# Kernel optimization log

Measured on AMD Instinct MI355X. Metric: run time of the kernel, lower is better.

Reference implementation:

```python
import jax, jax.numpy as jnp
import numpy as np

N_NODES = 100000
D_FEAT = 128            # per-embedding width; concat of 4 -> 512
INPUT_DIM = 4 * D_FEAT
HIDDEN_DIM = 64
N_SAMPLES = 250000


def _glorot(key, fan_in, fan_out):
    r = np.sqrt(6.0 / fan_in).astype(np.float32)
    return jax.random.uniform(key, (fan_in, fan_out), minval=-r, maxval=r, dtype=jnp.float32)


def setup_inputs() -> dict:
    key = jax.random.key(0)
    k1, k2, k3, k4, k5 = jax.random.split(key, 5)
    input1 = jax.random.normal(k1, (N_NODES, D_FEAT), dtype=jnp.float32)
    input2 = jax.random.normal(k2, (N_NODES, D_FEAT), dtype=jnp.float32)
    train_sample = jax.random.randint(k3, (N_SAMPLES, 2), 0, N_NODES, dtype=jnp.int64)
    w1 = _glorot(k4, INPUT_DIM, HIDDEN_DIM)
    b1 = jnp.zeros((HIDDEN_DIM,), dtype=jnp.float32)
    w2 = _glorot(k5, HIDDEN_DIM, 1)
    return {"input1": input1, "input2": input2, "train_sample": train_sample,
            "w1": w1, "b1": b1, "w2": w2}


def reference(input1, input2, train_sample, w1, b1, w2):
    src = train_sample[:, 0]
    dst = train_sample[:, 1]
    # four gathers + concat -> [E, 4*D_FEAT]
    h = jnp.concatenate([input1[src], input1[dst], input2[src], input2[dst]], axis=1)
    x = jax.nn.relu(h @ w1 + b1)          # [E, HIDDEN_DIM]
    return x @ w2                          # [E, 1]
```

## Files before the change

### kernel.cpp

```cpp
#include <hip/hip_runtime.h>
#include <hip/hip_bf16.h>

#define NN  100000
#define DF  128
#define HD  64
#define NS  250000


typedef __attribute__((ext_vector_type(8))) short bfrag;
typedef __attribute__((ext_vector_type(4))) float ffrag;

__device__ __forceinline__ unsigned short bf16bits(float f) {
    __hip_bfloat16 b = __float2bfloat16(f);
    return *(unsigned short*)&b;
}
__device__ __forceinline__ unsigned pack2(float a, float b) {
    return (unsigned)bf16bits(a) | ((unsigned)bf16bits(b) << 16);
}
__device__ __forceinline__ float bflo(unsigned u) {
    union { unsigned i; float f; } c; c.i = u << 16; return c.f;
}
__device__ __forceinline__ float bfhi(unsigned u) {
    union { unsigned i; float f; } c; c.i = u & 0xffff0000u; return c.f;
}
__device__ __forceinline__ void barrier_lgkm_only() {
    __builtin_amdgcn_s_waitcnt(0xC07F);
    __builtin_amdgcn_s_barrier();
}

__global__ __launch_bounds__(256) void prep_w1_kernel(
    const float* __restrict__ w1, const float* __restrict__ w2,
    unsigned short* __restrict__ Bf, unsigned short* __restrict__ w2bf)
{
    const int gid = blockIdx.x * 256 + threadIdx.x;
    if (gid >= 4096) {
        const int j = gid - 4096;
        if (j < HD) w2bf[j] = bf16bits(w2[j]);
        return;
    }
    const int lane = gid & 63;
    const int ks   = (gid >> 6) & 7;
    const int tn   = gid >> 9;

    const int n     = tn * 16 + (lane & 15);
    const int kbase = ks * 32 + (lane >> 4) * 8;
    const int col   = n & 63;

    uint4 u;
    unsigned p[4];
    #pragma unroll
    for (int jp = 0; jp < 4; ++jp) {
        float v[2];
        #pragma unroll
        for (int h = 0; h < 2; ++h) {
            const int k = kbase + jp * 2 + h;
            const int row = ((k >= 128) ? 256 : 0) + ((n >= 64) ? 128 : 0) + (k & 127);
            v[h] = w1[(size_t)row * HD + col];
        }
        p[jp] = pack2(v[0], v[1]);
    }
    u.x = p[0]; u.y = p[1]; u.z = p[2]; u.w = p[3];
    *(uint4*)(Bf + (size_t)gid * 8) = u;
}

#define NTILE 5
#define NBLK  (NN / (16 * NTILE))

__global__ __launch_bounds__(256) void node_gemm_mfma(
    const float* __restrict__ in1,
    const float* __restrict__ in2,
    const unsigned short* __restrict__ Bf,
    const float* __restrict__ b1,
    unsigned short* __restrict__ Pn)
{
    __shared__ unsigned short smem[8192 + 4 * 576];

    const int t    = threadIdx.x;
    const int lane = t & 63;
    const int w    = t >> 6;
    const int r  = t >> 4;
    const int qq = t & 15;

    bfrag bfr[2][8];
    #pragma unroll
    for (int ti = 0; ti < 2; ++ti) {
        const int tn = w * 2 + ti;
        #pragma unroll
        for (int ks = 0; ks < 8; ++ks)
            bfr[ti][ks] = *(const bfrag*)(Bf + ((size_t)(tn * 8 + ks) * 64 + lane) * 8);
    }
    float badd[2];
    #pragma unroll
    for (int ti = 0; ti < 2; ++ti) {
        const int nc = w * 32 + ti * 16 + (lane & 15);
        badd[ti] = (w < 2) ? b1[nc] : 0.f;
    }

    const int tile0 = blockIdx.x * NTILE;

    float4 f0, f1, f2, f3;
    {
        const int row = (tile0)*16 + r;
        const float* src = (qq < 8)
            ? in1 + (size_t)row * DF + qq * 16
            : in2 + (size_t)row * DF + (qq - 8) * 16;
        f0 = *(const float4*)(src);
        f1 = *(const float4*)(src + 4);
        f2 = *(const float4*)(src + 8);
        f3 = *(const float4*)(src + 12);
    }

    #pragma unroll
    for (int it = 0; it < NTILE; ++it) {
        const int m0 = (tile0 + it) * 16;

        float4 g0, g1, g2, g3;
        {
            const int nt  = (it + 1 < NTILE) ? (tile0 + it + 1) : tile0;
            const int row = nt * 16 + r;
            const float* src = (qq < 8)
                ? in1 + (size_t)row * DF + qq * 16
                : in2 + (size_t)row * DF + (qq - 8) * 16;
            g0 = *(const float4*)(src);
            g1 = *(const float4*)(src + 4);
            g2 = *(const float4*)(src + 8);
            g3 = *(const float4*)(src + 12);
        }

        unsigned short* abuf = &smem[(it & 1) * 4096];
        {
            uint4 u0, u1;
            u0.x = pack2(f0.x, f0.y); u0.y = pack2(f0.z, f0.w);
            u0.z = pack2(f1.x, f1.y); u0.w = pack2(f1.z, f1.w);
            u1.x = pack2(f2.x, f2.y); u1.y = pack2(f2.z, f2.w);
            u1.z = pack2(f3.x, f3.y); u1.w = pack2(f3.z, f3.w);
            const int g0i = qq * 2, g1i = qq * 2 + 1;
            *(uint4*)(&abuf[(g0i >> 2) * 512 + ((g0i & 3) * 16 + r) * 8]) = u0;
            *(uint4*)(&abuf[(g1i >> 2) * 512 + ((g1i & 3) * 16 + r) * 8]) = u1;
        }

        barrier_lgkm_only();

        ffrag acc[2] = {{0.f, 0.f, 0.f, 0.f}, {0.f, 0.f, 0.f, 0.f}};
        #pragma unroll
        for (int ks = 0; ks < 8; ++ks) {
            const bfrag af = *(const bfrag*)(&abuf[ks * 512 + lane * 8]);
            acc[0] = __builtin_amdgcn_mfma_f32_16x16x32_bf16(af, bfr[0][ks], acc[0], 0, 0, 0);
            acc[1] = __builtin_amdgcn_mfma_f32_16x16x32_bf16(af, bfr[1][ks], acc[1], 0, 0, 0);
        }

        {
            unsigned short* ep = &smem[8192 + w * 576];
            const int col = lane & 15;
            const int rq  = lane >> 4;
            #pragma unroll
            for (int ti = 0; ti < 2; ++ti) {
                #pragma unroll
                for (int reg = 0; reg < 4; ++reg)
                    ep[(rq * 4 + reg) * 36 + ti * 16 + col] =
                        bf16bits(acc[ti][reg] + badd[ti]);
            }
            const int rowm = lane >> 2;
            const int seg  = lane & 3;
            const uint4 u = *(const uint4*)(&ep[rowm * 36 + seg * 8]);
            *(uint4*)(Pn + (size_t)(m0 + rowm) * 128 + w * 32 + seg * 8) = u;
        }

        f0 = g0; f1 = g1; f2 = g2; f3 = g3;
    }
}

#define EBLK   1024
#define EPASS  4
__global__ __launch_bounds__(256) void edge_mlp_kernel(
    const unsigned short* __restrict__ Pn,
    const int*   __restrict__ ts,
    const unsigned short* __restrict__ w2bf,
    float* __restrict__ out)
{
    const int t = threadIdx.x;
    const int q = t & 3;
    const int g = t >> 2;

    const uint4 w0 = *(const uint4*)(w2bf + q * 16);
    const uint4 w1v = *(const uint4*)(w2bf + q * 16 + 8);

    const int2* ts2 = (const int2*)ts;

    int sr = blockIdx.x * 64 + g;
    int2 e = ts2[min(sr, NS - 1)];

    #pragma unroll
    for (int p = 0; p < EPASS; ++p) {
        const unsigned short* up = Pn + (size_t)e.x * 128 + q * 16;
        const unsigned short* vp = Pn + (size_t)e.y * 128 + 64 + q * 16;
        const uint4 u0 = *(const uint4*)(up);
        const uint4 u1 = *(const uint4*)(up + 8);
        const uint4 v0 = *(const uint4*)(vp);
        const uint4 v1 = *(const uint4*)(vp + 8);

        const int sr_n = sr + EBLK * 64;
        int2 e_n;
        if (p + 1 < EPASS) e_n = ts2[min(sr_n, NS - 1)];

        float acc = 0.f, x;
        x = bflo(u0.x) + bflo(v0.x); x = x > 0.f ? x : 0.f; acc += x * bflo(w0.x);
        x = bfhi(u0.x) + bfhi(v0.x); x = x > 0.f ? x : 0.f; acc += x * bfhi(w0.x);
        x = bflo(u0.y) + bflo(v0.y); x = x > 0.f ? x : 0.f; acc += x * bflo(w0.y);
        x = bfhi(u0.y) + bfhi(v0.y); x = x > 0.f ? x : 0.f; acc += x * bfhi(w0.y);
        x = bflo(u0.z) + bflo(v0.z); x = x > 0.f ? x : 0.f; acc += x * bflo(w0.z);
        x = bfhi(u0.z) + bfhi(v0.z); x = x > 0.f ? x : 0.f; acc += x * bfhi(w0.z);
        x = bflo(u0.w) + bflo(v0.w); x = x > 0.f ? x : 0.f; acc += x * bflo(w0.w);
        x = bfhi(u0.w) + bfhi(v0.w); x = x > 0.f ? x : 0.f; acc += x * bfhi(w0.w);
        x = bflo(u1.x) + bflo(v1.x); x = x > 0.f ? x : 0.f; acc += x * bflo(w1v.x);
        x = bfhi(u1.x) + bfhi(v1.x); x = x > 0.f ? x : 0.f; acc += x * bfhi(w1v.x);
        x = bflo(u1.y) + bflo(v1.y); x = x > 0.f ? x : 0.f; acc += x * bflo(w1v.y);
        x = bfhi(u1.y) + bfhi(v1.y); x = x > 0.f ? x : 0.f; acc += x * bfhi(w1v.y);
        x = bflo(u1.z) + bflo(v1.z); x = x > 0.f ? x : 0.f; acc += x * bflo(w1v.z);
        x = bfhi(u1.z) + bfhi(v1.z); x = x > 0.f ? x : 0.f; acc += x * bfhi(w1v.z);
        x = bflo(u1.w) + bflo(v1.w); x = x > 0.f ? x : 0.f; acc += x * bflo(w1v.w);
        x = bfhi(u1.w) + bfhi(v1.w); x = x > 0.f ? x : 0.f; acc += x * bfhi(w1v.w);

        acc += __shfl_xor(acc, 1);
        acc += __shfl_xor(acc, 2);
        if (q == 0 && sr < NS) out[sr] = acc;

        sr = sr_n;
        e  = e_n;
    }
}

extern "C" void kernel_launch(void* const* d_in, const int* in_sizes, int n_in,
                              void* d_out, int out_size, void* d_ws, size_t ws_size,
                              hipStream_t stream) {
    const float* in1 = (const float*)d_in[0];
    const float* in2 = (const float*)d_in[1];
    const int*   ts  = (const int*)  d_in[2];
    const float* w1  = (const float*)d_in[3];
    const float* b1  = (const float*)d_in[4];
    const float* w2  = (const float*)d_in[5];
    float* out = (float*)d_out;

    unsigned short* Pn = (unsigned short*)d_ws;
    const size_t Pbytes = (size_t)NN * 128 * sizeof(unsigned short);
    unsigned short* Bf;
    unsigned short* w2bf;
    if (ws_size >= Pbytes + 65536 + 128) {
        Bf   = (unsigned short*)((char*)d_ws + Pbytes);
        w2bf = (unsigned short*)((char*)d_ws + Pbytes + 65536);
    } else {
        Bf   = (unsigned short*)d_out;
        w2bf = (unsigned short*)((char*)d_out + 65536);
    }

    prep_w1_kernel<<<17, 256, 0, stream>>>(w1, w2, Bf, w2bf);
    node_gemm_mfma<<<NBLK, 256, 0, stream>>>(in1, in2, Bf, b1, Pn);
    edge_mlp_kernel<<<EBLK, 256, 0, stream>>>(Pn, ts, w2bf, out);
}
```

Before: 147.8 us.

## Coalesce node GEMM input loads, swizzle LDS layout, shrink tiles per block

The node GEMM now loads each 16-row tile of in1/in2 as fully contiguous float4 spans across the block instead of 64-byte per-thread row chunks. It writes to LDS with an XOR swizzle so the MFMA fragment reads avoid bank conflicts. NTILE drops from 5 to 2, which gives more blocks and removes the wasted final prefetch. The cost is more per-block setup, including reloading the B fragments into registers for fewer tiles per block.

```diff
diff --git a/kernel.cpp b/kernel.cpp
--- a/kernel.cpp
+++ b/kernel.cpp
@@ -63,7 +63,7 @@
     *(uint4*)(Bf + (size_t)gid * 8) = u;
 }
 
-#define NTILE 5
+#define NTILE 2
 #define NBLK  (NN / (16 * NTILE))
 
 __global__ __launch_bounds__(256) void node_gemm_mfma(
@@ -78,8 +78,6 @@
     const int t    = threadIdx.x;
     const int lane = t & 63;
     const int w    = t >> 6;
-    const int r  = t >> 4;
-    const int qq = t & 15;
 
     bfrag bfr[2][8];
     #pragma unroll
@@ -96,47 +94,52 @@
         badd[ti] = (w < 2) ? b1[nc] : 0.f;
     }
 
+    int ldsoff[4];
+    #pragma unroll
+    for (int i = 0; i < 4; ++i) {
+        const int p  = (i & 1) * 256 + t;
+        const int m  = p >> 5;
+        const int c  = p & 31;
+        const int k  = ((i >> 1) ? 128 : 0) + c * 4;
+        const int ks = k >> 5;
+        const int g  = (k >> 3) & 3;
+        const int l  = m + 16 * g;
+        ldsoff[i] = ks * 512 + ((l * 8) ^ (g << 3)) + (k & 7);
+    }
+    const int lane_off = (lane * 8) ^ ((lane >> 4) << 3);
+
     const int tile0 = blockIdx.x * NTILE;
 
-    float4 f0, f1, f2, f3;
+    float4 cur[4], nxt[4];
     {
-        const int row = (tile0)*16 + r;
-        const float* src = (qq < 8)
-            ? in1 + (size_t)row * DF + qq * 16
-            : in2 + (size_t)row * DF + (qq - 8) * 16;
-        f0 = *(const float4*)(src);
-        f1 = *(const float4*)(src + 4);
-        f2 = *(const float4*)(src + 8);
-        f3 = *(const float4*)(src + 12);
+        const float* a1 = in1 + (size_t)tile0 * 16 * DF;
+        const float* a2 = in2 + (size_t)tile0 * 16 * DF;
+        cur[0] = *(const float4*)(a1 + t * 4);
+        cur[1] = *(const float4*)(a1 + 1024 + t * 4);
+        cur[2] = *(const float4*)(a2 + t * 4);
+        cur[3] = *(const float4*)(a2 + 1024 + t * 4);
     }
 
     #pragma unroll
     for (int it = 0; it < NTILE; ++it) {
         const int m0 = (tile0 + it) * 16;
 
-        float4 g0, g1, g2, g3;
-        {
-            const int nt  = (it + 1 < NTILE) ? (tile0 + it + 1) : tile0;
-            const int row = nt * 16 + r;
-            const float* src = (qq < 8)
-                ? in1 + (size_t)row * DF + qq * 16
-                : in2 + (size_t)row * DF + (qq - 8) * 16;
-            g0 = *(const float4*)(src);
-            g1 = *(const float4*)(src + 4);
-            g2 = *(const float4*)(src + 8);
-            g3 = *(const float4*)(src + 12);
+        if (it + 1 < NTILE) {
+            const float* a1 = in1 + (size_t)(m0 + 16) * DF;
+            const float* a2 = in2 + (size_t)(m0 + 16) * DF;
+            nxt[0] = *(const float4*)(a1 + t * 4);
+            nxt[1] = *(const float4*)(a1 + 1024 + t * 4);
+            nxt[2] = *(const float4*)(a2 + t * 4);
+            nxt[3] = *(const float4*)(a2 + 1024 + t * 4);
         }
 
         unsigned short* abuf = &smem[(it & 1) * 4096];
-        {
-            uint4 u0, u1;
-            u0.x = pack2(f0.x, f0.y); u0.y = pack2(f0.z, f0.w);
-            u0.z = pack2(f1.x, f1.y); u0.w = pack2(f1.z, f1.w);
-            u1.x = pack2(f2.x, f2.y); u1.y = pack2(f2.z, f2.w);
-            u1.z = pack2(f3.x, f3.y); u1.w = pack2(f3.z, f3.w);
-            const int g0i = qq * 2, g1i = qq * 2 + 1;
-            *(uint4*)(&abuf[(g0i >> 2) * 512 + ((g0i & 3) * 16 + r) * 8]) = u0;
-            *(uint4*)(&abuf[(g1i >> 2) * 512 + ((g1i & 3) * 16 + r) * 8]) = u1;
+        #pragma unroll
+        for (int i = 0; i < 4; ++i) {
+            uint2 u;
+            u.x = pack2(cur[i].x, cur[i].y);
+            u.y = pack2(cur[i].z, cur[i].w);
+            *(uint2*)(&abuf[ldsoff[i]]) = u;
         }
 
         barrier_lgkm_only();
@@ -144,7 +147,7 @@
         ffrag acc[2] = {{0.f, 0.f, 0.f, 0.f}, {0.f, 0.f, 0.f, 0.f}};
         #pragma unroll
         for (int ks = 0; ks < 8; ++ks) {
-            const bfrag af = *(const bfrag*)(&abuf[ks * 512 + lane * 8]);
+            const bfrag af = *(const bfrag*)(&abuf[ks * 512 + lane_off]);
             acc[0] = __builtin_amdgcn_mfma_f32_16x16x32_bf16(af, bfr[0][ks], acc[0], 0, 0, 0);
             acc[1] = __builtin_amdgcn_mfma_f32_16x16x32_bf16(af, bfr[1][ks], acc[1], 0, 0, 0);
         }
@@ -166,7 +169,8 @@
             *(uint4*)(Pn + (size_t)(m0 + rowm) * 128 + w * 32 + seg * 8) = u;
         }
 
-        f0 = g0; f1 = g1; f2 = g2; f3 = g3;
+        #pragma unroll
+        for (int i = 0; i < 4; ++i) cur[i] = nxt[i];
     }
 }
 
```

Measured after the change: 146.3 us. No clear change (-1.0%).
